# Kernel tuning notes

Measured on AMD Instinct MI355X. Metric: run time of the kernel, lower is better.

Reference implementation:

```python
import jax, jax.numpy as jnp
import numpy as np

# ---- static skeleton topology (SMPL-like, 24 joints) ----
TOPOLOGY = np.array([0, 0, 0, 0, 1, 2, 3, 4, 5, 6, 7, 8, 9, 9, 9, 12, 13, 14, 16, 17, 18, 19, 20, 21])
NEIGHBOR_DIST = 1
EE_ID = [10, 11, 15, 22, 23]


def _neighbor_lists():
    J = len(TOPOLOGY)
    INF = 100000
    mat = np.full((J, J), INF, dtype=np.int64)
    for i, p in enumerate(TOPOLOGY.tolist()):
        mat[i, p] = mat[p, i] = 1
    np.fill_diagonal(mat, 0)
    for k in range(J):  # Floyd-Warshall, J=24 so trivial cost
        mat = np.minimum(mat, mat[:, k:k + 1] + mat[k:k + 1, :])
    nl = [list(np.where(mat[i] <= NEIGHBOR_DIST)[0]) for i in range(J)]
    root = sorted(set(nl[0]) | set(EE_ID) | {0})  # root gets end-effectors appended
    nl[0] = root
    return nl

# Flattened gather indices: concat of all per-joint neighbor lists (75 rows total).
# Because kernel height is 1 (no mixing across the joint axis), conv(concat) == concat(conv),
# so one gather + one conv reproduces the per-joint conv+concat loop exactly.
ALL_IDX = np.concatenate([np.asarray(n, dtype=np.int32) for n in _neighbor_lists()])

B, C_IN, C_OUT, J, T = 32, 16, 16, 24, 4096


def setup_inputs() -> dict:
    key = jax.random.key(0)
    kx, kw = jax.random.split(key)
    x = jax.random.normal(kx, (B, C_IN, J, T), dtype=jnp.float32)
    # Conv2d weight (OIHW) with kernel (1, 3), plus bias
    W = jax.random.normal(kw, (C_OUT, C_IN, 1, 3), dtype=jnp.float32) * 0.05
    b = jnp.zeros((C_OUT,), dtype=jnp.float32)
    return {"x": x, "W": W, "b": b}


def reference(x, W, b):
    idx = jnp.asarray(ALL_IDX)
    xg = x[:, :, idx, :]  # [B, C_in, 75, T] gathered neighbor rows
    out = jax.lax.conv_general_dilated(
        xg, W,
        window_strides=(1, 1),
        padding=((0, 0), (1, 1)),  # no joint padding, temporal pad 1
        dimension_numbers=("NCHW", "OIHW", "NCHW"),
    )
    return out + b[None, :, None, None]  # [B, C_out, 75, T]
```

## Files before the change

kernel.cpp:

```cpp
#include <hip/hip_runtime.h>

#define T_DIM 4096
#define J_DIM 24
#define NCI 16
#define NCO 16
#define G_DIM 75
#define WAVE_T 256
#define TILE_T (WAVE_T * 4)

__device__ const int d_nrep[J_DIM] = {4,3,3,3,3,3,3,3,3,5,3,3,3,3,3,3,3,3,3,3,3,3,3,3};
__device__ const int d_repl[J_DIM][5] = {
  {0, 9, 12, 15, -1},
  {1, 10, 18, -1, -1},
  {2, 13, 21, -1, -1},
  {3, 16, 24, -1, -1},
  {11, 19, 27, -1, -1},
  {14, 22, 30, -1, -1},
  {17, 25, 33, -1, -1},
  {20, 28, 38, -1, -1},
  {23, 31, 40, -1, -1},
  {26, 34, 42, 45, 48},
  {4, 29, 39, -1, -1},
  {5, 32, 41, -1, -1},
  {35, 43, 51, -1, -1},
  {36, 46, 53, -1, -1},
  {37, 49, 56, -1, -1},
  {6, 44, 52, -1, -1},
  {47, 54, 59, -1, -1},
  {50, 57, 62, -1, -1},
  {55, 60, 65, -1, -1},
  {58, 63, 68, -1, -1},
  {61, 66, 71, -1, -1},
  {64, 69, 73, -1, -1},
  {7, 67, 72, -1, -1},
  {8, 70, 74, -1, -1},
};

__global__ __launch_bounds__(256, 4) void skel_conv(
    const float* __restrict__ x, const float* __restrict__ W,
    const float* __restrict__ bias, float* __restrict__ out) {
  const int tile = blockIdx.x;
  const int j    = blockIdx.y;
  const int b    = blockIdx.z;
  const int tid  = (int)threadIdx.x;
  const int lane = tid & 63;
  const int wv = __builtin_amdgcn_readfirstlane(tid >> 6);

  const int t0 = tile * TILE_T + wv * WAVE_T + lane * 4;

  float4 acc[NCO];
#pragma unroll
  for (int co = 0; co < NCO; ++co) {
    const float bb = bias[co];
    acc[co] = make_float4(bb, bb, bb, bb);
  }

#pragma unroll 2
  for (int ci = 0; ci < NCI; ++ci) {
    const float* xp = x + (((size_t)b * NCI + ci) * J_DIM + j) * T_DIM;
    const float4 v = *(const float4*)(xp + t0);
    float xm1 = __shfl_up(v.w, 1);
    float xp4 = __shfl_down(v.x, 1);
    if (lane == 0)  xm1 = (t0 > 0) ? xp[t0 - 1] : 0.f;
    if (lane == 63) xp4 = (t0 + 4 < T_DIM) ? xp[t0 + 4] : 0.f;

#pragma unroll
    for (int co = 0; co < NCO; ++co) {
      const float w0 = W[(co * NCI + ci) * 3 + 0];
      const float w1 = W[(co * NCI + ci) * 3 + 1];
      const float w2 = W[(co * NCI + ci) * 3 + 2];
      acc[co].x = fmaf(xm1, w0, fmaf(v.x, w1, fmaf(v.y, w2, acc[co].x)));
      acc[co].y = fmaf(v.x, w0, fmaf(v.y, w1, fmaf(v.z, w2, acc[co].y)));
      acc[co].z = fmaf(v.y, w0, fmaf(v.z, w1, fmaf(v.w, w2, acc[co].z)));
      acc[co].w = fmaf(v.z, w0, fmaf(v.w, w1, fmaf(xp4, w2, acc[co].w)));
    }
  }

  __syncthreads();

  const int nrep = d_nrep[j];
  float* ob = out + (size_t)b * NCO * G_DIM * T_DIM + t0;
#pragma unroll
  for (int co = 0; co < NCO; ++co) {
    float* oc = ob + (size_t)co * (G_DIM * T_DIM);
    for (int r = 0; r < nrep; ++r) {
      const int g = d_repl[j][r];
      *(float4*)(oc + (size_t)g * T_DIM) = acc[co];
    }
  }
}

extern "C" void kernel_launch(void* const* d_in, const int* in_sizes, int n_in,
                              void* d_out, int out_size, void* d_ws, size_t ws_size,
                              hipStream_t stream) {
  const float* x    = (const float*)d_in[0];
  const float* W    = (const float*)d_in[1];
  const float* bias = (const float*)d_in[2];
  float* out = (float*)d_out;

  dim3 grid(T_DIM / TILE_T, J_DIM, 32);
  dim3 block(256);
  skel_conv<<<grid, block, 0, stream>>>(x, W, bias, out);
}
```

Baseline: 177.3 us.

## Load all input channels upfront and interleave per-channel compute with stores

Swaps the loop order. All 16 input-channel float4 values and their halos are loaded into registers before any compute starts. Each output channel is then computed in full and stored right away, instead of holding 16 accumulators until the end. This issues all global loads at once for more memory-level parallelism, lets stores overlap with compute, and drops the unnecessary __syncthreads. It trades accumulator registers for input registers, so register pressure is roughly unchanged.

```diff
diff --git a/kernel.cpp b/kernel.cpp
--- a/kernel.cpp
+++ b/kernel.cpp
@@ -7,6 +7,7 @@
 #define G_DIM 75
 #define WAVE_T 256
 #define TILE_T (WAVE_T * 4)
+#define ROW_STRIDE ((size_t)J_DIM * T_DIM)
 
 __device__ const int d_nrep[J_DIM] = {4,3,3,3,3,3,3,3,3,5,3,3,3,3,3,3,3,3,3,3,3,3,3,3};
 __device__ const int d_repl[J_DIM][5] = {
@@ -47,45 +48,51 @@
   const int wv = __builtin_amdgcn_readfirstlane(tid >> 6);
 
   const int t0 = tile * TILE_T + wv * WAVE_T + lane * 4;
+  const float* xb = x + ((size_t)b * NCI * J_DIM + j) * T_DIM;
 
-  float4 acc[NCO];
+  float4 xr[NCI];
 #pragma unroll
-  for (int co = 0; co < NCO; ++co) {
-    const float bb = bias[co];
-    acc[co] = make_float4(bb, bb, bb, bb);
+  for (int ci = 0; ci < NCI; ++ci)
+    xr[ci] = *(const float4*)(xb + ci * ROW_STRIDE + t0);
+
+  float xm[NCI], xp[NCI];
+#pragma unroll
+  for (int ci = 0; ci < NCI; ++ci) {
+    xm[ci] = __shfl_up(xr[ci].w, 1);
+    xp[ci] = __shfl_down(xr[ci].x, 1);
   }
-
-#pragma unroll 2
-  for (int ci = 0; ci < NCI; ++ci) {
-    const float* xp = x + (((size_t)b * NCI + ci) * J_DIM + j) * T_DIM;
-    const float4 v = *(const float4*)(xp + t0);
-    float xm1 = __shfl_up(v.w, 1);
-    float xp4 = __shfl_down(v.x, 1);
-    if (lane == 0)  xm1 = (t0 > 0) ? xp[t0 - 1] : 0.f;
-    if (lane == 63) xp4 = (t0 + 4 < T_DIM) ? xp[t0 + 4] : 0.f;
-
+  if (lane == 0) {
 #pragma unroll
-    for (int co = 0; co < NCO; ++co) {
-      const float w0 = W[(co * NCI + ci) * 3 + 0];
-      const float w1 = W[(co * NCI + ci) * 3 + 1];
-      const float w2 = W[(co * NCI + ci) * 3 + 2];
-      acc[co].x = fmaf(xm1, w0, fmaf(v.x, w1, fmaf(v.y, w2, acc[co].x)));
-      acc[co].y = fmaf(v.x, w0, fmaf(v.y, w1, fmaf(v.z, w2, acc[co].y)));
-      acc[co].z = fmaf(v.y, w0, fmaf(v.z, w1, fmaf(v.w, w2, acc[co].z)));
-      acc[co].w = fmaf(v.z, w0, fmaf(v.w, w1, fmaf(xp4, w2, acc[co].w)));
-    }
+    for (int ci = 0; ci < NCI; ++ci)
+      xm[ci] = (t0 > 0) ? xb[ci * ROW_STRIDE + t0 - 1] : 0.f;
   }
-
-  __syncthreads();
+  if (lane == 63) {
+#pragma unroll
+    for (int ci = 0; ci < NCI; ++ci)
+      xp[ci] = (t0 + 4 < T_DIM) ? xb[ci * ROW_STRIDE + t0 + 4] : 0.f;
+  }
 
   const int nrep = d_nrep[j];
   float* ob = out + (size_t)b * NCO * G_DIM * T_DIM + t0;
 #pragma unroll
   for (int co = 0; co < NCO; ++co) {
+    const float bb = bias[co];
+    float4 a = make_float4(bb, bb, bb, bb);
+#pragma unroll
+    for (int ci = 0; ci < NCI; ++ci) {
+      const float w0 = W[(co * NCI + ci) * 3 + 0];
+      const float w1 = W[(co * NCI + ci) * 3 + 1];
+      const float w2 = W[(co * NCI + ci) * 3 + 2];
+      const float4 v = xr[ci];
+      a.x = fmaf(xm[ci], w0, fmaf(v.x, w1, fmaf(v.y, w2, a.x)));
+      a.y = fmaf(v.x,    w0, fmaf(v.y, w1, fmaf(v.z, w2, a.y)));
+      a.z = fmaf(v.y,    w0, fmaf(v.z, w1, fmaf(v.w, w2, a.z)));
+      a.w = fmaf(v.z,    w0, fmaf(v.w, w1, fmaf(xp[ci], w2, a.w)));
+    }
     float* oc = ob + (size_t)co * (G_DIM * T_DIM);
     for (int r = 0; r < nrep; ++r) {
       const int g = d_repl[j][r];
-      *(float4*)(oc + (size_t)g * T_DIM) = acc[co];
+      *(float4*)(oc + (size_t)g * T_DIM) = a;
     }
   }
 }
```

Measured after the change: 494.6 us. +179.0%, slower.
